# Optimization experiments

Measured on AMD Instinct MI355X. Metric: run time of the kernel, lower is better.

The kernel has to match this reference:

```python
import jax, jax.numpy as jnp
import numpy as np

DIM = 33


def setup_inputs() -> dict:
    key = jax.random.key(0)
    k1, k2 = jax.random.split(key)
    # LUT param: (3, dim, dim, dim). Module inits to ones; use uniform values
    # so the reference exercises non-trivial gathers.
    lut = jax.random.uniform(k1, (3, DIM, DIM, DIM), dtype=jnp.float32)
    # Input image batch (B, C=3, W, H), values in [0, 1).
    x = jax.random.uniform(k2, (8, 3, 1920, 1080), dtype=jnp.float32)
    return {"lut": lut, "x": x}


def reference(lut, x):
    # Faithful JAX port of the trilinear.forward CUDA kernel used by Lut3D.
    dim = lut.shape[-1]
    binsize = 1.000001 / (dim - 1)
    xb = x / binsize  # (B, 3, W, H)
    idx = jnp.clip(jnp.floor(xb).astype(jnp.int32), 0, dim - 2)
    frac = xb - idx.astype(x.dtype)
    # channel 0 = r, 1 = g, 2 = b; flat id = r + g*dim + b*dim^2 -> LUT[c, b, g, r]
    rid, gid, bid = idx[:, 0], idx[:, 1], idx[:, 2]  # each (B, W, H)
    rd, gd, bd = frac[:, 0], frac[:, 1], frac[:, 2]

    def corner(db, dg, dr):
        # gather 8 neighboring LUT cells -> (3, B, W, H)
        return lut[:, bid + db, gid + dg, rid + dr]

    w000 = (1 - rd) * (1 - gd) * (1 - bd)
    w100 = rd * (1 - gd) * (1 - bd)
    w010 = (1 - rd) * gd * (1 - bd)
    w110 = rd * gd * (1 - bd)
    w001 = (1 - rd) * (1 - gd) * bd
    w101 = rd * (1 - gd) * bd
    w011 = (1 - rd) * gd * bd
    w111 = rd * gd * bd

    out = (corner(0, 0, 0) * w000 + corner(0, 0, 1) * w100
           + corner(0, 1, 0) * w010 + corner(0, 1, 1) * w110
           + corner(1, 0, 0) * w001 + corner(1, 0, 1) * w101
           + corner(1, 1, 0) * w011 + corner(1, 1, 1) * w111)  # (3, B, W, H)
    return jnp.transpose(out, (1, 0, 2, 3))  # (B, 3, W, H)
```

## Files before the change

kernel.cpp:

```cpp
#include <hip/hip_runtime.h>
#include <stdint.h>

#define DIM 33
#define D2 (DIM * DIM)
#define NENT (DIM * DIM * DIM)
#define HW 2073600
#define NIMG 8
#define HW4 (HW / 4)
#define QP (NIMG * HW4)
#define BLK 1024
#define NBLK 256
#define STRIDE (BLK * NBLK)
#define STRIDE2 (2 * STRIDE)

typedef float f32x4 __attribute__((ext_vector_type(4)));
typedef uint32_t u32x4 __attribute__((ext_vector_type(4)));

__device__ __forceinline__ float lerpf(float a, float b, float t) {
    return fmaf(t, b - a, a);
}

__global__ __launch_bounds__(256) void build_packed10(const float* __restrict__ lut,
                                                      uint32_t* __restrict__ T) {
    int e = blockIdx.x * 256 + threadIdx.x;
    if (e >= NENT) return;
    uint32_t q0 = (uint32_t)(lut[e] * 1023.f + 0.5f);
    uint32_t q1 = (uint32_t)(lut[NENT + e] * 1023.f + 0.5f);
    uint32_t q2 = (uint32_t)(lut[2 * NENT + e] * 1023.f + 0.5f);
    T[e] = q0 | (q1 << 10) | (q2 << 20);
}

#define U0(v) ((float)((v) & 1023u))
#define U1(v) ((float)(((v) >> 10) & 1023u))
#define U2(v) ((float)((v) >> 20))

__device__ __forceinline__ void loadq(const float* __restrict__ x, int j, bool valid,
                                      f32x4& R, f32x4& G, f32x4& B) {
    if (valid) {
        int img = j / HW4;
        int i = (j - img * HW4) * 4;
        const float* xp = x + (size_t)img * 3 * HW + i;
        R = *(const f32x4*)xp;
        G = *(const f32x4*)(xp + HW);
        B = *(const f32x4*)(xp + 2 * HW);
    } else {
        R = f32x4{0.f, 0.f, 0.f, 0.f};
        G = f32x4{0.f, 0.f, 0.f, 0.f};
        B = f32x4{0.f, 0.f, 0.f, 0.f};
    }
}

__device__ __forceinline__ void idxfrac(float r, float g, float b,
                                        int& base, float& rd, float& gd, float& bd) {
    const float inv = 32.0f / 1.000001f;
    float xr = r * inv;
    float xg = g * inv;
    float xb = b * inv;
    int ri = (int)xr; ri = ri > DIM - 2 ? DIM - 2 : ri;
    int gi = (int)xg; gi = gi > DIM - 2 ? DIM - 2 : gi;
    int bi = (int)xb; bi = bi > DIM - 2 ? DIM - 2 : bi;
    rd = xr - (float)ri;
    gd = xg - (float)gi;
    bd = xb - (float)bi;
    base = (bi * DIM + gi) * DIM + ri;
}

__device__ __forceinline__ void interp(const uint32_t (&v)[8], float rd, float gd, float bd,
                                       float& o0, float& o1, float& o2) {
    const float qs = 1.0f / 1023.0f;
    {
        float q00 = lerpf(U0(v[0]), U0(v[1]), rd);
        float q01 = lerpf(U0(v[2]), U0(v[3]), rd);
        float q10 = lerpf(U0(v[4]), U0(v[5]), rd);
        float q11 = lerpf(U0(v[6]), U0(v[7]), rd);
        o0 = lerpf(lerpf(q00, q01, gd), lerpf(q10, q11, gd), bd) * qs;
    }
    {
        float q00 = lerpf(U1(v[0]), U1(v[1]), rd);
        float q01 = lerpf(U1(v[2]), U1(v[3]), rd);
        float q10 = lerpf(U1(v[4]), U1(v[5]), rd);
        float q11 = lerpf(U1(v[6]), U1(v[7]), rd);
        o1 = lerpf(lerpf(q00, q01, gd), lerpf(q10, q11, gd), bd) * qs;
    }
    {
        float q00 = lerpf(U2(v[0]), U2(v[1]), rd);
        float q01 = lerpf(U2(v[2]), U2(v[3]), rd);
        float q10 = lerpf(U2(v[4]), U2(v[5]), rd);
        float q11 = lerpf(U2(v[6]), U2(v[7]), rd);
        o2 = lerpf(lerpf(q00, q01, gd), lerpf(q10, q11, gd), bd) * qs;
    }
}

__global__ __launch_bounds__(1024) void lut3d_lds(const float* __restrict__ x,
                                                  const uint32_t* __restrict__ T,
                                                  float* __restrict__ out) {
    __shared__ __align__(16) uint32_t L[NENT];

    {
        const u32x4* T4 = (const u32x4*)T;
        u32x4* L4 = (u32x4*)L;
        for (int e = threadIdx.x; e < NENT / 4; e += BLK) L4[e] = T4[e];
        if (threadIdx.x == 0) L[NENT - 1] = T[NENT - 1];
    }

    const int j0 = blockIdx.x * BLK + threadIdx.x;

    f32x4 RA, GA, BA, RB, GB, BB;
    loadq(x, j0, true, RA, GA, BA);
    loadq(x, j0 + STRIDE, true, RB, GB, BB);

    __syncthreads();

#pragma unroll 1
    for (int p = 0; p < 8; ++p) {
        const int jA = j0 + p * STRIDE2;
        const int jB = jA + STRIDE;
        const bool vB = (jB < QP);

        int base[8];
        float rd[8], gd[8], bd[8];
#pragma unroll
        for (int k = 0; k < 4; ++k)
            idxfrac(RA[k], GA[k], BA[k], base[k], rd[k], gd[k], bd[k]);
#pragma unroll
        for (int k = 0; k < 4; ++k)
            idxfrac(RB[k], GB[k], BB[k], base[4 + k], rd[4 + k], gd[4 + k], bd[4 + k]);

        uint32_t v[8][8];
#pragma unroll
        for (int k = 0; k < 8; ++k) {
            const int b0 = base[k];
            v[k][0] = L[b0];            v[k][1] = L[b0 + 1];
            v[k][2] = L[b0 + DIM];      v[k][3] = L[b0 + DIM + 1];
            v[k][4] = L[b0 + D2];       v[k][5] = L[b0 + D2 + 1];
            v[k][6] = L[b0 + D2 + DIM]; v[k][7] = L[b0 + D2 + DIM + 1];
        }

        if (p < 7) {
            const int jA2 = jA + STRIDE2;
            loadq(x, jA2, true, RA, GA, BA);
            loadq(x, jA2 + STRIDE, jA2 + STRIDE < QP, RB, GB, BB);
        }

        float o[8][3];
#pragma unroll
        for (int k = 0; k < 8; ++k)
            interp(v[k], rd[k], gd[k], bd[k], o[k][0], o[k][1], o[k][2]);

        {
            const int img = jA / HW4;
            const int i = (jA - img * HW4) * 4;
            float* op = out + (size_t)img * 3 * HW + i;
            f32x4 v0 = {o[0][0], o[1][0], o[2][0], o[3][0]};
            f32x4 v1 = {o[0][1], o[1][1], o[2][1], o[3][1]};
            f32x4 v2 = {o[0][2], o[1][2], o[2][2], o[3][2]};
            __builtin_nontemporal_store(v0, (f32x4*)op);
            __builtin_nontemporal_store(v1, (f32x4*)(op + HW));
            __builtin_nontemporal_store(v2, (f32x4*)(op + 2 * HW));
        }
        if (vB) {
            const int img = jB / HW4;
            const int i = (jB - img * HW4) * 4;
            float* op = out + (size_t)img * 3 * HW + i;
            f32x4 v0 = {o[4][0], o[5][0], o[6][0], o[7][0]};
            f32x4 v1 = {o[4][1], o[5][1], o[6][1], o[7][1]};
            f32x4 v2 = {o[4][2], o[5][2], o[6][2], o[7][2]};
            __builtin_nontemporal_store(v0, (f32x4*)op);
            __builtin_nontemporal_store(v1, (f32x4*)(op + HW));
            __builtin_nontemporal_store(v2, (f32x4*)(op + 2 * HW));
        }
    }
}

__global__ __launch_bounds__(256) void lut3d_direct(const float* __restrict__ x,
                                                    const float* __restrict__ lut,
                                                    float* __restrict__ out) {
    const int img = blockIdx.y;
    const int i = (blockIdx.x * 256 + threadIdx.x) * 4;
    const float* xp = x + (size_t)img * 3 * HW + i;
    f32x4 Rv = *(const f32x4*)xp;
    f32x4 Gv = *(const f32x4*)(xp + HW);
    f32x4 Bv = *(const f32x4*)(xp + 2 * HW);
    float o0[4], o1[4], o2[4];
    const float inv = 32.0f / 1.000001f;
#pragma unroll
    for (int k = 0; k < 4; ++k) {
        float xr = Rv[k] * inv;
        float xg = Gv[k] * inv;
        float xb = Bv[k] * inv;
        int ri = (int)xr; ri = ri < 0 ? 0 : (ri > DIM - 2 ? DIM - 2 : ri);
        int gi = (int)xg; gi = gi < 0 ? 0 : (gi > DIM - 2 ? DIM - 2 : gi);
        int bi = (int)xb; bi = bi < 0 ? 0 : (bi > DIM - 2 ? DIM - 2 : bi);
        float rd = xr - (float)ri;
        float gd = xg - (float)gi;
        float bd = xb - (float)bi;
        int base = (bi * DIM + gi) * DIM + ri;
        float oc[3];
#pragma unroll
        for (int c = 0; c < 3; ++c) {
            const float* Lp = lut + c * NENT + base;
            float v000 = Lp[0],        v001 = Lp[1];
            float v010 = Lp[DIM],      v011 = Lp[DIM + 1];
            float v100 = Lp[D2],       v101 = Lp[D2 + 1];
            float v110 = Lp[D2 + DIM], v111 = Lp[D2 + DIM + 1];
            float q0 = lerpf(v000, v001, rd);
            float q1 = lerpf(v010, v011, rd);
            float q2 = lerpf(v100, v101, rd);
            float q3 = lerpf(v110, v111, rd);
            float p0 = lerpf(q0, q1, gd);
            float p1 = lerpf(q2, q3, gd);
            oc[c] = lerpf(p0, p1, bd);
        }
        o0[k] = oc[0]; o1[k] = oc[1]; o2[k] = oc[2];
    }
    float* op = out + (size_t)img * 3 * HW + i;
    f32x4 v0 = {o0[0], o0[1], o0[2], o0[3]};
    f32x4 v1 = {o1[0], o1[1], o1[2], o1[3]};
    f32x4 v2 = {o2[0], o2[1], o2[2], o2[3]};
    *(f32x4*)op = v0;
    *(f32x4*)(op + HW) = v1;
    *(f32x4*)(op + 2 * HW) = v2;
}

extern "C" void kernel_launch(void* const* d_in, const int* in_sizes, int n_in,
                              void* d_out, int out_size, void* d_ws, size_t ws_size,
                              hipStream_t stream) {
    const float* lut = (const float*)d_in[0];
    const float* x   = (const float*)d_in[1];
    float* out = (float*)d_out;

    if (ws_size >= (size_t)NENT * 4) {
        uint32_t* T = (uint32_t*)d_ws;
        build_packed10<<<(NENT + 255) / 256, 256, 0, stream>>>(lut, T);
        lut3d_lds<<<NBLK, BLK, 0, stream>>>(x, T, out);
    } else {
        const dim3 grid(HW / 4 / 256, NIMG);
        lut3d_direct<<<grid, dim3(256), 0, stream>>>(x, lut, out);
    }
}
```

Baseline: 376.2 us.

## Software-pipeline LDS gathers and interpolation across A/B halves in LUT kernel

Restructures the main loop so the LDS gathers for the next A group are issued while the B group is interpolated and stored, with the first A gather hoisted before the loop. Interpolation and the store are fused into a per-group helper that writes each channel as soon as it is computed. It also adds a minimum-blocks hint of 4 to launch bounds. Together these aim to hide LDS gather latency behind ALU work, but holding two full sets of 32 gathered words and the register cap implied by the new hint raise register pressure and the risk of spills.

Measured after the change: 375.8 us. No clear change (-0.1%).

```diff
diff --git a/kernel.cpp b/kernel.cpp
--- a/kernel.cpp
+++ b/kernel.cpp
@@ -65,35 +65,64 @@
     base = (bi * DIM + gi) * DIM + ri;
 }
 
-__device__ __forceinline__ void interp(const uint32_t (&v)[8], float rd, float gd, float bd,
-                                       float& o0, float& o1, float& o2) {
+__device__ __forceinline__ void gather8(const uint32_t* __restrict__ L, int b0,
+                                        uint32_t (&v)[8]) {
+    v[0] = L[b0];            v[1] = L[b0 + 1];
+    v[2] = L[b0 + DIM];      v[3] = L[b0 + DIM + 1];
+    v[4] = L[b0 + D2];       v[5] = L[b0 + D2 + 1];
+    v[6] = L[b0 + D2 + DIM]; v[7] = L[b0 + D2 + DIM + 1];
+}
+
+__device__ __forceinline__ void interp_store(float* __restrict__ out, int j,
+                                             const uint32_t (&v)[4][8],
+                                             const float (&rd)[4],
+                                             const float (&gd)[4],
+                                             const float (&bd)[4]) {
     const float qs = 1.0f / 1023.0f;
-    {
-        float q00 = lerpf(U0(v[0]), U0(v[1]), rd);
-        float q01 = lerpf(U0(v[2]), U0(v[3]), rd);
-        float q10 = lerpf(U0(v[4]), U0(v[5]), rd);
-        float q11 = lerpf(U0(v[6]), U0(v[7]), rd);
-        o0 = lerpf(lerpf(q00, q01, gd), lerpf(q10, q11, gd), bd) * qs;
-    }
-    {
-        float q00 = lerpf(U1(v[0]), U1(v[1]), rd);
-        float q01 = lerpf(U1(v[2]), U1(v[3]), rd);
-        float q10 = lerpf(U1(v[4]), U1(v[5]), rd);
-        float q11 = lerpf(U1(v[6]), U1(v[7]), rd);
-        o1 = lerpf(lerpf(q00, q01, gd), lerpf(q10, q11, gd), bd) * qs;
-    }
-    {
-        float q00 = lerpf(U2(v[0]), U2(v[1]), rd);
-        float q01 = lerpf(U2(v[2]), U2(v[3]), rd);
-        float q10 = lerpf(U2(v[4]), U2(v[5]), rd);
-        float q11 = lerpf(U2(v[6]), U2(v[7]), rd);
-        o2 = lerpf(lerpf(q00, q01, gd), lerpf(q10, q11, gd), bd) * qs;
-    }
-}
-
-__global__ __launch_bounds__(1024) void lut3d_lds(const float* __restrict__ x,
-                                                  const uint32_t* __restrict__ T,
-                                                  float* __restrict__ out) {
+    const int img = j / HW4;
+    const int i = (j - img * HW4) * 4;
+    float* op = out + (size_t)img * 3 * HW + i;
+    {
+        f32x4 o;
+#pragma unroll
+        for (int k = 0; k < 4; ++k) {
+            float q00 = lerpf(U0(v[k][0]), U0(v[k][1]), rd[k]);
+            float q01 = lerpf(U0(v[k][2]), U0(v[k][3]), rd[k]);
+            float q10 = lerpf(U0(v[k][4]), U0(v[k][5]), rd[k]);
+            float q11 = lerpf(U0(v[k][6]), U0(v[k][7]), rd[k]);
+            o[k] = lerpf(lerpf(q00, q01, gd[k]), lerpf(q10, q11, gd[k]), bd[k]) * qs;
+        }
+        __builtin_nontemporal_store(o, (f32x4*)op);
+    }
+    {
+        f32x4 o;
+#pragma unroll
+        for (int k = 0; k < 4; ++k) {
+            float q00 = lerpf(U1(v[k][0]), U1(v[k][1]), rd[k]);
+            float q01 = lerpf(U1(v[k][2]), U1(v[k][3]), rd[k]);
+            float q10 = lerpf(U1(v[k][4]), U1(v[k][5]), rd[k]);
+            float q11 = lerpf(U1(v[k][6]), U1(v[k][7]), rd[k]);
+            o[k] = lerpf(lerpf(q00, q01, gd[k]), lerpf(q10, q11, gd[k]), bd[k]) * qs;
+        }
+        __builtin_nontemporal_store(o, (f32x4*)(op + HW));
+    }
+    {
+        f32x4 o;
+#pragma unroll
+        for (int k = 0; k < 4; ++k) {
+            float q00 = lerpf(U2(v[k][0]), U2(v[k][1]), rd[k]);
+            float q01 = lerpf(U2(v[k][2]), U2(v[k][3]), rd[k]);
+            float q10 = lerpf(U2(v[k][4]), U2(v[k][5]), rd[k]);
+            float q11 = lerpf(U2(v[k][6]), U2(v[k][7]), rd[k]);
+            o[k] = lerpf(lerpf(q00, q01, gd[k]), lerpf(q10, q11, gd[k]), bd[k]) * qs;
+        }
+        __builtin_nontemporal_store(o, (f32x4*)(op + 2 * HW));
+    }
+}
+
+__global__ __launch_bounds__(1024, 4) void lut3d_lds(const float* __restrict__ x,
+                                                     const uint32_t* __restrict__ T,
+                                                     float* __restrict__ out) {
     __shared__ __align__(16) uint32_t L[NENT];
 
     {
@@ -111,64 +140,50 @@
 
     __syncthreads();
 
+    uint32_t vA[4][8], vB[4][8];
+    float rdA[4], gdA[4], bdA[4], rdB[4], gdB[4], bdB[4];
+    {
+        int baseA[4];
+#pragma unroll
+        for (int k = 0; k < 4; ++k)
+            idxfrac(RA[k], GA[k], BA[k], baseA[k], rdA[k], gdA[k], bdA[k]);
+#pragma unroll
+        for (int k = 0; k < 4; ++k) gather8(L, baseA[k], vA[k]);
+    }
+
 #pragma unroll 1
     for (int p = 0; p < 8; ++p) {
         const int jA = j0 + p * STRIDE2;
         const int jB = jA + STRIDE;
-        const bool vB = (jB < QP);
-
-        int base[8];
-        float rd[8], gd[8], bd[8];
-#pragma unroll
-        for (int k = 0; k < 4; ++k)
-            idxfrac(RA[k], GA[k], BA[k], base[k], rd[k], gd[k], bd[k]);
-#pragma unroll
-        for (int k = 0; k < 4; ++k)
-            idxfrac(RB[k], GB[k], BB[k], base[4 + k], rd[4 + k], gd[4 + k], bd[4 + k]);
-
-        uint32_t v[8][8];
-#pragma unroll
-        for (int k = 0; k < 8; ++k) {
-            const int b0 = base[k];
-            v[k][0] = L[b0];            v[k][1] = L[b0 + 1];
-            v[k][2] = L[b0 + DIM];      v[k][3] = L[b0 + DIM + 1];
-            v[k][4] = L[b0 + D2];       v[k][5] = L[b0 + D2 + 1];
-            v[k][6] = L[b0 + D2 + DIM]; v[k][7] = L[b0 + D2 + DIM + 1];
-        }
-
-        if (p < 7) {
-            const int jA2 = jA + STRIDE2;
-            loadq(x, jA2, true, RA, GA, BA);
-            loadq(x, jA2 + STRIDE, jA2 + STRIDE < QP, RB, GB, BB);
-        }
-
-        float o[8][3];
-#pragma unroll
-        for (int k = 0; k < 8; ++k)
-            interp(v[k], rd[k], gd[k], bd[k], o[k][0], o[k][1], o[k][2]);
 
         {
-            const int img = jA / HW4;
-            const int i = (jA - img * HW4) * 4;
-            float* op = out + (size_t)img * 3 * HW + i;
-            f32x4 v0 = {o[0][0], o[1][0], o[2][0], o[3][0]};
-            f32x4 v1 = {o[0][1], o[1][1], o[2][1], o[3][1]};
-            f32x4 v2 = {o[0][2], o[1][2], o[2][2], o[3][2]};
-            __builtin_nontemporal_store(v0, (f32x4*)op);
-            __builtin_nontemporal_store(v1, (f32x4*)(op + HW));
-            __builtin_nontemporal_store(v2, (f32x4*)(op + 2 * HW));
-        }
-        if (vB) {
-            const int img = jB / HW4;
-            const int i = (jB - img * HW4) * 4;
-            float* op = out + (size_t)img * 3 * HW + i;
-            f32x4 v0 = {o[4][0], o[5][0], o[6][0], o[7][0]};
-            f32x4 v1 = {o[4][1], o[5][1], o[6][1], o[7][1]};
-            f32x4 v2 = {o[4][2], o[5][2], o[6][2], o[7][2]};
-            __builtin_nontemporal_store(v0, (f32x4*)op);
-            __builtin_nontemporal_store(v1, (f32x4*)(op + HW));
-            __builtin_nontemporal_store(v2, (f32x4*)(op + 2 * HW));
-        }
+            int baseB[4];
+#pragma unroll
+            for (int k = 0; k < 4; ++k)
+                idxfrac(RB[k], GB[k], BB[k], baseB[k], rdB[k], gdB[k], bdB[k]);
+#pragma unroll
+            for (int k = 0; k < 4; ++k) gather8(L, baseB[k], vB[k]);
+        }
+
+        f32x4 RA2, GA2, BA2, RB2, GB2, BB2;
+        const bool pv = (p < 7);
+        loadq(x, jA + STRIDE2, pv, RA2, GA2, BA2);
+        loadq(x, jB + STRIDE2, pv && (jB + STRIDE2 < QP), RB2, GB2, BB2);
+
+        interp_store(out, jA, vA, rdA, gdA, bdA);
+
+        {
+            int baseA[4];
+#pragma unroll
+            for (int k = 0; k < 4; ++k)
+                idxfrac(RA2[k], GA2[k], BA2[k], baseA[k], rdA[k], gdA[k], bdA[k]);
+#pragma unroll
+            for (int k = 0; k < 4; ++k) gather8(L, baseA[k], vA[k]);
+        }
+
+        if (jB < QP) interp_store(out, jB, vB, rdB, gdB, bdB);
+
+        RB = RB2; GB = GB2; BB = BB2;
     }
 }
 
```
